# Optimization experiments

Measured on AMD Instinct MI355X. Metric: run time of the kernel, lower is better.

The kernel has to match this reference:

```python
import jax, jax.numpy as jnp
import numpy as np

N_EC, N_DG, N_CA3, N_CA1 = 100000, 400000, 120000, 100000
N_I_DG, N_I_CA3, N_I_CA1 = 10000, 3000, 2000
PP_NNZ, MF_NNZ, RC_NNZ, SC_NNZ = 10000000, 8000000, 6000000, 6000000
T, DT = 4, 0.5
A, B = 0.02, 0.2                      # Izhikevich a,b (same across subfields)
TAU_I, THR_I, INH_GAIN = 0.9, 1.0, 2.0  # inhibitory LIF params
IZH_CD = {'ec': (-65.0, 8.0), 'dg': (-65.0, 8.0), 'ca3': (-55.0, 4.0), 'ca1': (-65.0, 6.0)}


def _edges(key, n_src, n_tgt, nnz):
    # COO edge list matching init_sparse_projection: vals ~ N(0.5, 0.1), clamped >= 0
    k1, k2, k3 = jax.random.split(key, 3)
    src = jax.random.randint(k1, (nnz,), 0, n_src, dtype=jnp.int32)
    tgt = jax.random.randint(k2, (nnz,), 0, n_tgt, dtype=jnp.int32)
    val = jnp.clip(jax.random.normal(k3, (nnz,), jnp.float32) * 0.1 + 0.5, 0.0, None)
    return src, tgt, val


def _hetero(key, n, c, d):
    # per-neuron heterogeneity: c += 10 r^2, d -= 4 r^2, r ~ U(0,1)
    r = jax.random.uniform(key, (n,), jnp.float32)
    return jnp.float32(c) + 10.0 * r ** 2, jnp.float32(d) - 4.0 * r ** 2


def setup_inputs() -> dict:
    key = jax.random.key(0)
    ks = jax.random.split(key, 9)
    pp_src, pp_tgt, pp_val = _edges(ks[0], N_EC, N_DG, PP_NNZ)    # perforant path
    mf_src, mf_tgt, mf_val = _edges(ks[1], N_DG, N_CA3, MF_NNZ)   # mossy fibers
    rc_src, rc_tgt, rc_val = _edges(ks[2], N_CA3, N_CA3, RC_NNZ)  # CA3 recurrent
    sc_src, sc_tgt, sc_val = _edges(ks[3], N_CA3, N_CA1, SC_NNZ)  # Schaffer collaterals
    ec_c, ec_d = _hetero(ks[4], N_EC, *IZH_CD['ec'])
    dg_c, dg_d = _hetero(ks[5], N_DG, *IZH_CD['dg'])
    ca3_c, ca3_d = _hetero(ks[6], N_CA3, *IZH_CD['ca3'])
    ca1_c, ca1_d = _hetero(ks[7], N_CA1, *IZH_CD['ca1'])
    drive = jax.random.uniform(ks[8], (T, N_EC), jnp.float32) * 20.0  # input current, strong enough to spike
    return dict(drive=drive,
                pp_src=pp_src, pp_tgt=pp_tgt, pp_val=pp_val,
                mf_src=mf_src, mf_tgt=mf_tgt, mf_val=mf_val,
                rc_src=rc_src, rc_tgt=rc_tgt, rc_val=rc_val,
                sc_src=sc_src, sc_tgt=sc_tgt, sc_val=sc_val,
                ec_c=ec_c, ec_d=ec_d, dg_c=dg_c, dg_d=dg_d,
                ca3_c=ca3_c, ca3_d=ca3_d, ca1_c=ca1_c, ca1_d=ca1_d)


def reference(drive, pp_src, pp_tgt, pp_val, mf_src, mf_tgt, mf_val,
              rc_src, rc_tgt, rc_val, sc_src, sc_tgt, sc_val,
              ec_c, ec_d, dg_c, dg_d, ca3_c, ca3_d, ca1_c, ca1_d):

    def transmit(spk, src, tgt, val, n_tgt):
        # sparse_transmit: W^T @ spikes as gather + segment-scatter-add
        return jax.ops.segment_sum(val * spk[src], tgt, num_segments=n_tgt)

    def izh(v, u, c, d, I):
        v = jnp.clip(v + (0.04 * v * v + 5.0 * v + 140.0 - u + I) * DT, -90.0, 40.0)
        u = u + A * (B * v - u) * DT  # du uses post-update clamped v, as in torch
        s = (v >= 30.0).astype(jnp.float32)
        return jnp.where(s > 0, c, v), jnp.where(s > 0, u + d, u), s

    def lif(v, inp):
        v = TAU_I * v + (1.0 - TAU_I) * inp
        s = (v >= THR_I).astype(jnp.float32)
        return jnp.where(s > 0, 0.0, v), s

    def step(carry, I_ec):
        (ec_v, ec_u, dg_v, dg_u, c3_v, c3_u, c1_v, c1_u,
         c3_s, iv_dg, iv_c3, iv_c1) = carry
        # EC -> perforant path -> DG
        ec_v, ec_u, ec_s = izh(ec_v, ec_u, ec_c, ec_d, I_ec)
        dg_I = transmit(ec_s, pp_src, pp_tgt, pp_val, N_DG)
        iv_dg, is_dg = lif(iv_dg, jnp.full((N_I_DG,), dg_I.mean()))
        dg_v, dg_u, dg_s = izh(dg_v, dg_u, dg_c, dg_d, dg_I - INH_GAIN * is_dg.mean())
        # DG -> mossy fibers + CA3 recurrent -> CA3
        c3_I = (transmit(dg_s, mf_src, mf_tgt, mf_val, N_CA3)
                + transmit(c3_s, rc_src, rc_tgt, rc_val, N_CA3))
        iv_c3, is_c3 = lif(iv_c3, jnp.full((N_I_CA3,), c3_I.mean()))
        c3_v, c3_u, c3_s = izh(c3_v, c3_u, ca3_c, ca3_d, c3_I - INH_GAIN * is_c3.mean())
        # CA3 -> Schaffer collaterals -> CA1
        c1_I = transmit(c3_s, sc_src, sc_tgt, sc_val, N_CA1)
        iv_c1, is_c1 = lif(iv_c1, jnp.full((N_I_CA1,), c1_I.mean()))
        c1_v, c1_u, c1_s = izh(c1_v, c1_u, ca1_c, ca1_d, c1_I - INH_GAIN * is_c1.mean())
        carry = (ec_v, ec_u, dg_v, dg_u, c3_v, c3_u, c1_v, c1_u,
                 c3_s, iv_dg, iv_c3, iv_c1)
        return carry, c1_s

    f32 = jnp.float32
    init = (jnp.full((N_EC,), -65.0, f32), jnp.full((N_EC,), B * -65.0, f32),
            jnp.full((N_DG,), -65.0, f32), jnp.full((N_DG,), B * -65.0, f32),
            jnp.full((N_CA3,), -65.0, f32), jnp.full((N_CA3,), B * -65.0, f32),
            jnp.full((N_CA1,), -65.0, f32), jnp.full((N_CA1,), B * -65.0, f32),
            jnp.zeros((N_CA3,), f32),
            jnp.zeros((N_I_DG,), f32), jnp.zeros((N_I_CA3,), f32), jnp.zeros((N_I_CA1,), f32))
    carry, _ = jax.lax.scan(step, init, drive)
    return carry[6]  # final CA1 membrane potential, shape (N_CA1,)
```

## Files before the change

### kernel.cpp

```cpp
#include <hip/hip_runtime.h>


#define N_EC  100000
#define N_DG  400000
#define N_CA3 120000
#define N_CA1 100000

constexpr int PP_NNZ = 10000000, MF_NNZ = 8000000, RC_NNZ = 6000000, SC_NNZ = 6000000;
constexpr int T_STEPS = 4;

enum : size_t {
  OFF_EC_V = 0,
  OFF_EC_U = OFF_EC_V + N_EC,
  OFF_DG_V = OFF_EC_U + N_EC,
  OFF_DG_U = OFF_DG_V + N_DG,
  OFF_C3_V = OFF_DG_U + N_DG,
  OFF_C3_U = OFF_C3_V + N_CA3,
  OFF_C1_V = OFF_C3_U + N_CA3,
  OFF_C1_U = OFF_C1_V + N_CA1,
  OFF_DG_I = OFF_C1_U + N_CA1,
  OFF_C3_I = OFF_DG_I + N_DG,
  OFF_C1_I = OFF_C3_I + N_CA3,
  OFF_SCAL = OFF_C1_I + N_CA1,
  OFF_FLAG = OFF_SCAL + 64,
  OFF_MASK = OFF_FLAG + 64,
};
enum : size_t {
  MW_EC = 0,    MW_EC_N = 1600,
  MW_DG = 1600, MW_DG_N = 6272,
  MW_C3 = 7872, MW_C3_N = 1900,
  MW_TOT = 9772,
};

__global__ __launch_bounds__(256)
void init_kernel(float* __restrict__ ws) {
  int i0 = blockIdx.x * blockDim.x + threadIdx.x;
  int stride = gridDim.x * blockDim.x;
  int* flags = (int*)(ws + OFF_FLAG);
  unsigned long long* c3m = (unsigned long long*)(ws + OFF_MASK) + MW_C3;
  for (int j = i0; j < N_DG; j += stride) {
    ws[OFF_DG_V + j] = -65.0f; ws[OFF_DG_U + j] = -13.0f; ws[OFF_DG_I + j] = 0.0f;
    if (j < N_EC)  { ws[OFF_EC_V + j] = -65.0f; ws[OFF_EC_U + j] = -13.0f; }
    if (j < N_CA3) { ws[OFF_C3_V + j] = -65.0f; ws[OFF_C3_U + j] = -13.0f; ws[OFF_C3_I + j] = 0.0f; }
    if (j < N_CA1) { ws[OFF_C1_V + j] = -65.0f; ws[OFF_C1_U + j] = -13.0f; ws[OFF_C1_I + j] = 0.0f; }
    if (j < 64) ws[OFF_SCAL + j] = 0.0f;
    if (j < 16) flags[j] = 0;
    if (j < (int)MW_C3_N) c3m[j] = 0ull;
  }
}

__global__ __launch_bounds__(256)
void transmit_kernel(const int* __restrict__ src, const int* __restrict__ tgt,
                     const float* __restrict__ val,
                     const unsigned long long* __restrict__ mask,
                     float* __restrict__ I, float* __restrict__ sum_slot,
                     const int* __restrict__ flag, int nnz4)
{
  if (*flag == 0) return;
  float local = 0.0f;
  const int stride = gridDim.x * blockDim.x;
  for (int i = blockIdx.x * blockDim.x + threadIdx.x; i < nnz4; i += stride) {
    const int4   s4 = reinterpret_cast<const int4*>(src)[i];
    const int4   t4 = reinterpret_cast<const int4*>(tgt)[i];
    const float4 v4 = reinterpret_cast<const float4*>(val)[i];
    const int   ss[4] = {s4.x, s4.y, s4.z, s4.w};
    const int   tt[4] = {t4.x, t4.y, t4.z, t4.w};
    const float vv[4] = {v4.x, v4.y, v4.z, v4.w};
#pragma unroll
    for (int k = 0; k < 4; ++k) {
      if ((mask[ss[k] >> 6] >> (ss[k] & 63)) & 1ull) {
        atomicAdd(&I[tt[k]], vv[k]);
        local += vv[k];
      }
    }
  }
  for (int off = 32; off > 0; off >>= 1) local += __shfl_down(local, off);
  __shared__ float red[4];
  if ((threadIdx.x & 63) == 0) red[threadIdx.x >> 6] = local;
  __syncthreads();
  if (threadIdx.x == 0) {
    float bs = red[0] + red[1] + red[2] + red[3];
    if (bs != 0.0f) atomicAdd(sum_slot, bs);
  }
}

__device__ __forceinline__ void izh_step(float& vv, float& uu, float I,
                                         float c, float d, bool& s) {
  vv = vv + (0.04f * vv * vv + 5.0f * vv + 140.0f - uu + I) * 0.5f;
  vv = fminf(fmaxf(vv, -90.0f), 40.0f);
  uu = uu + 0.02f * (0.2f * vv - uu) * 0.5f;
  s = (vv >= 30.0f);
  if (s) { vv = c; uu = uu + d; }
}

__global__ __launch_bounds__(256)
void izh_ec_kernel(float* __restrict__ v, float* __restrict__ u,
                   const float* __restrict__ c, const float* __restrict__ d,
                   const float* __restrict__ drive,
                   unsigned long long* __restrict__ mask,
                   int* __restrict__ flag, int n)
{
  int i = blockIdx.x * blockDim.x + threadIdx.x;
  bool s = false;
  if (i < n) {
    float vv = v[i], uu = u[i];
    izh_step(vv, uu, drive[i], c[i], d[i], s);
    v[i] = vv; u[i] = uu;
  }
  unsigned long long m = __ballot(s);
  if ((threadIdx.x & 63) == 0) {
    mask[i >> 6] = m;
    if (m) atomicOr(flag, 1);
  }
}

__global__ __launch_bounds__(256)
void izh_lif_kernel(float* __restrict__ v, float* __restrict__ u,
                    const float* __restrict__ c, const float* __restrict__ d,
                    float* __restrict__ Ibuf,
                    const float* __restrict__ sum_slot,
                    const float* __restrict__ iv_prev, float* __restrict__ iv_next,
                    float inv_n,
                    unsigned long long* __restrict__ mask, int* __restrict__ flag,
                    float* __restrict__ out, int n)
{
  float mean = (*sum_slot) * inv_n;
  float ivn  = 0.9f * (*iv_prev) + 0.1f * mean;
  bool  lif_s = (ivn >= 1.0f);
  float inh   = lif_s ? 2.0f : 0.0f;
  if (blockIdx.x == 0 && threadIdx.x == 0) *iv_next = lif_s ? 0.0f : ivn;

  int i = blockIdx.x * blockDim.x + threadIdx.x;
  bool s = false;
  if (i < n) {
    float vv = v[i], uu = u[i];
    float I = Ibuf[i] - inh;
    Ibuf[i] = 0.0f;
    izh_step(vv, uu, I, c[i], d[i], s);
    v[i] = vv; u[i] = uu;
    if (out) out[i] = vv;
  }
  if (mask) {
    unsigned long long m = __ballot(s);
    if ((threadIdx.x & 63) == 0) {
      mask[i >> 6] = m;
      if (m) atomicOr(flag, 1);
    }
  }
}

extern "C" void kernel_launch(void* const* d_in, const int* in_sizes, int n_in,
                              void* d_out, int out_size, void* d_ws, size_t ws_size,
                              hipStream_t stream) {
  const float* drive  = (const float*)d_in[0];
  const int *pp_src = (const int*)d_in[1], *pp_tgt = (const int*)d_in[2];
  const float* pp_val = (const float*)d_in[3];
  const int *mf_src = (const int*)d_in[4], *mf_tgt = (const int*)d_in[5];
  const float* mf_val = (const float*)d_in[6];
  const int *rc_src = (const int*)d_in[7], *rc_tgt = (const int*)d_in[8];
  const float* rc_val = (const float*)d_in[9];
  const int *sc_src = (const int*)d_in[10], *sc_tgt = (const int*)d_in[11];
  const float* sc_val = (const float*)d_in[12];
  const float *ec_c = (const float*)d_in[13], *ec_d = (const float*)d_in[14];
  const float *dg_c = (const float*)d_in[15], *dg_d = (const float*)d_in[16];
  const float *c3_c = (const float*)d_in[17], *c3_d = (const float*)d_in[18];
  const float *c1_c = (const float*)d_in[19], *c1_d = (const float*)d_in[20];

  float* ws = (float*)d_ws;
  float* ec_v = ws + OFF_EC_V;  float* ec_u = ws + OFF_EC_U;
  float* dg_v = ws + OFF_DG_V;  float* dg_u = ws + OFF_DG_U;
  float* c3_v = ws + OFF_C3_V;  float* c3_u = ws + OFF_C3_U;
  float* c1_v = ws + OFF_C1_V;  float* c1_u = ws + OFF_C1_U;
  float* dg_I = ws + OFF_DG_I;  float* c3_I = ws + OFF_C3_I;  float* c1_I = ws + OFF_C1_I;
  float* scal = ws + OFF_SCAL;
  int*   flags = (int*)(ws + OFF_FLAG);
  unsigned long long* mbase = (unsigned long long*)(ws + OFF_MASK);
  unsigned long long* ec_m = mbase + MW_EC;
  unsigned long long* dg_m = mbase + MW_DG;
  unsigned long long* c3_m = mbase + MW_C3;

  float* out = (float*)d_out;
  auto grid = [](int n) { return (n + 255) / 256; };

  init_kernel<<<grid(N_DG), 256, 0, stream>>>(ws);

  for (int t = 0; t < T_STEPS; ++t) {
    float* sum_dg = &scal[t * 3 + 0];
    float* sum_c3 = &scal[t * 3 + 1];
    float* sum_c1 = &scal[t * 3 + 2];
    int* f_ec = &flags[t * 3 + 0];
    int* f_dg = &flags[t * 3 + 1];
    int* f_c3 = &flags[t * 3 + 2];
    int* f_c3_prev = (t == 0) ? &flags[15] : &flags[(t - 1) * 3 + 2];

    izh_ec_kernel<<<grid(N_EC), 256, 0, stream>>>(
        ec_v, ec_u, ec_c, ec_d, drive + (size_t)t * N_EC, ec_m, f_ec, N_EC);
    transmit_kernel<<<1024, 256, 0, stream>>>(
        pp_src, pp_tgt, pp_val, ec_m, dg_I, sum_dg, f_ec, PP_NNZ / 4);
    izh_lif_kernel<<<grid(N_DG), 256, 0, stream>>>(
        dg_v, dg_u, dg_c, dg_d, dg_I, sum_dg, &scal[16 + t], &scal[16 + t + 1],
        1.0f / (float)N_DG, dg_m, f_dg, nullptr, N_DG);
    transmit_kernel<<<1024, 256, 0, stream>>>(
        mf_src, mf_tgt, mf_val, dg_m, c3_I, sum_c3, f_dg, MF_NNZ / 4);
    transmit_kernel<<<1024, 256, 0, stream>>>(
        rc_src, rc_tgt, rc_val, c3_m, c3_I, sum_c3, f_c3_prev, RC_NNZ / 4);
    izh_lif_kernel<<<grid(N_CA3), 256, 0, stream>>>(
        c3_v, c3_u, c3_c, c3_d, c3_I, sum_c3, &scal[21 + t], &scal[21 + t + 1],
        1.0f / (float)N_CA3, c3_m, f_c3, nullptr, N_CA3);
    transmit_kernel<<<1024, 256, 0, stream>>>(
        sc_src, sc_tgt, sc_val, c3_m, c1_I, sum_c1, f_c3, SC_NNZ / 4);
    izh_lif_kernel<<<grid(N_CA1), 256, 0, stream>>>(
        c1_v, c1_u, c1_c, c1_d, c1_I, sum_c1, &scal[26 + t], &scal[26 + t + 1],
        1.0f / (float)N_CA1, nullptr, nullptr, out, N_CA1);
  }
}
```

Baseline: 326.0 us.

## Fuse whole simulation into one cooperative persistent kernel with grid syncs

Replaces the roughly 29 separate kernel launches per call with a single cooperative kernel of 512 blocks. Neuron state (v, u, c, d) lives in registers across time steps, and stages are separated by grid.sync instead of kernel boundaries. Grid syncs and zero-current reads are skipped when no spikes occurred. This is meant to remove launch overhead and repeated state loads and stores. In exchange it uses fewer threads for the atomic-heavy scatter loops, which can lower memory-level parallelism, and grid-wide barriers carry their own cost.

Measured after the change: 1.022 ms. +213.4%, slower.

```diff
diff --git a/kernel.cpp b/kernel.cpp
--- a/kernel.cpp
+++ b/kernel.cpp
@@ -1,4 +1,7 @@
 #include <hip/hip_runtime.h>
+#include <hip/hip_cooperative_groups.h>
+
+namespace cg = cooperative_groups;
 
 
 #define N_EC  100000
@@ -8,58 +11,51 @@
 
 constexpr int PP_NNZ = 10000000, MF_NNZ = 8000000, RC_NNZ = 6000000, SC_NNZ = 6000000;
 constexpr int T_STEPS = 4;
-
-enum : size_t {
-  OFF_EC_V = 0,
-  OFF_EC_U = OFF_EC_V + N_EC,
-  OFF_DG_V = OFF_EC_U + N_EC,
-  OFF_DG_U = OFF_DG_V + N_DG,
-  OFF_C3_V = OFF_DG_U + N_DG,
-  OFF_C3_U = OFF_C3_V + N_CA3,
-  OFF_C1_V = OFF_C3_U + N_CA3,
-  OFF_C1_U = OFF_C1_V + N_CA1,
-  OFF_DG_I = OFF_C1_U + N_CA1,
-  OFF_C3_I = OFF_DG_I + N_DG,
-  OFF_C1_I = OFF_C3_I + N_CA3,
-  OFF_SCAL = OFF_C1_I + N_CA1,
-  OFF_FLAG = OFF_SCAL + 64,
-  OFF_MASK = OFF_FLAG + 64,
+constexpr int NBLK = 512, TPB = 256;
+constexpr int NTH  = NBLK * TPB;
+constexpr int DGS  = (N_DG + NTH - 1) / NTH;
+
+constexpr size_t OFF_DG_I = 0;
+constexpr size_t OFF_C3_I = OFF_DG_I + N_DG;
+constexpr size_t OFF_C1_I = OFF_C3_I + N_CA3;
+constexpr size_t OFF_SUMS = OFF_C1_I + N_CA1;
+constexpr size_t OFF_FLAG = OFF_SUMS + 16;
+constexpr size_t OFF_MASK = OFF_FLAG + 16;
+constexpr size_t MW_EC = 0,    MW_EC_N = 1564;
+constexpr size_t MW_DG = 1564, MW_DG_N = 6250;
+constexpr size_t MW_C3 = 7814, MW_C3_N = 1876;
+
+struct SimParams {
+  const float* drive;
+  const int *pp_src, *pp_tgt; const float* pp_val;
+  const int *mf_src, *mf_tgt; const float* mf_val;
+  const int *rc_src, *rc_tgt; const float* rc_val;
+  const int *sc_src, *sc_tgt; const float* sc_val;
+  const float *ec_c, *ec_d, *dg_c, *dg_d, *c3_c, *c3_d, *c1_c, *c1_d;
+  float* out; float* ws;
 };
-enum : size_t {
-  MW_EC = 0,    MW_EC_N = 1600,
-  MW_DG = 1600, MW_DG_N = 6272,
-  MW_C3 = 7872, MW_C3_N = 1900,
-  MW_TOT = 9772,
-};
-
-__global__ __launch_bounds__(256)
-void init_kernel(float* __restrict__ ws) {
-  int i0 = blockIdx.x * blockDim.x + threadIdx.x;
-  int stride = gridDim.x * blockDim.x;
-  int* flags = (int*)(ws + OFF_FLAG);
-  unsigned long long* c3m = (unsigned long long*)(ws + OFF_MASK) + MW_C3;
-  for (int j = i0; j < N_DG; j += stride) {
-    ws[OFF_DG_V + j] = -65.0f; ws[OFF_DG_U + j] = -13.0f; ws[OFF_DG_I + j] = 0.0f;
-    if (j < N_EC)  { ws[OFF_EC_V + j] = -65.0f; ws[OFF_EC_U + j] = -13.0f; }
-    if (j < N_CA3) { ws[OFF_C3_V + j] = -65.0f; ws[OFF_C3_U + j] = -13.0f; ws[OFF_C3_I + j] = 0.0f; }
-    if (j < N_CA1) { ws[OFF_C1_V + j] = -65.0f; ws[OFF_C1_U + j] = -13.0f; ws[OFF_C1_I + j] = 0.0f; }
-    if (j < 64) ws[OFF_SCAL + j] = 0.0f;
-    if (j < 16) flags[j] = 0;
-    if (j < (int)MW_C3_N) c3m[j] = 0ull;
-  }
-}
-
-__global__ __launch_bounds__(256)
-void transmit_kernel(const int* __restrict__ src, const int* __restrict__ tgt,
-                     const float* __restrict__ val,
-                     const unsigned long long* __restrict__ mask,
-                     float* __restrict__ I, float* __restrict__ sum_slot,
-                     const int* __restrict__ flag, int nnz4)
-{
-  if (*flag == 0) return;
+
+__device__ __forceinline__ void izh_step(float& vv, float& uu, float I,
+                                         float c, float d, bool& s) {
+  vv = vv + (0.04f * vv * vv + 5.0f * vv + 140.0f - uu + I) * 0.5f;
+  vv = fminf(fmaxf(vv, -90.0f), 40.0f);
+  uu = uu + 0.02f * (0.2f * vv - uu) * 0.5f;
+  s = (vv >= 30.0f);
+  if (s) { vv = c; uu = uu + d; }
+}
+
+__device__ __forceinline__ float wave_sum(float x) {
+  for (int o = 32; o > 0; o >>= 1) x += __shfl_down(x, o);
+  return x;
+}
+
+__device__ void transmit(const int* __restrict__ src, const int* __restrict__ tgt,
+                         const float* __restrict__ val, int nnz4,
+                         const unsigned long long* __restrict__ mask,
+                         float* __restrict__ I, float* __restrict__ sum_slot,
+                         int tid) {
   float local = 0.0f;
-  const int stride = gridDim.x * blockDim.x;
-  for (int i = blockIdx.x * blockDim.x + threadIdx.x; i < nnz4; i += stride) {
+  for (int i = tid; i < nnz4; i += NTH) {
     const int4   s4 = reinterpret_cast<const int4*>(src)[i];
     const int4   t4 = reinterpret_cast<const int4*>(tgt)[i];
     const float4 v4 = reinterpret_cast<const float4*>(val)[i];
@@ -74,143 +70,155 @@
       }
     }
   }
-  for (int off = 32; off > 0; off >>= 1) local += __shfl_down(local, off);
-  __shared__ float red[4];
-  if ((threadIdx.x & 63) == 0) red[threadIdx.x >> 6] = local;
-  __syncthreads();
-  if (threadIdx.x == 0) {
-    float bs = red[0] + red[1] + red[2] + red[3];
-    if (bs != 0.0f) atomicAdd(sum_slot, bs);
-  }
-}
-
-__device__ __forceinline__ void izh_step(float& vv, float& uu, float I,
-                                         float c, float d, bool& s) {
-  vv = vv + (0.04f * vv * vv + 5.0f * vv + 140.0f - uu + I) * 0.5f;
-  vv = fminf(fmaxf(vv, -90.0f), 40.0f);
-  uu = uu + 0.02f * (0.2f * vv - uu) * 0.5f;
-  s = (vv >= 30.0f);
-  if (s) { vv = c; uu = uu + d; }
-}
-
-__global__ __launch_bounds__(256)
-void izh_ec_kernel(float* __restrict__ v, float* __restrict__ u,
-                   const float* __restrict__ c, const float* __restrict__ d,
-                   const float* __restrict__ drive,
-                   unsigned long long* __restrict__ mask,
-                   int* __restrict__ flag, int n)
-{
-  int i = blockIdx.x * blockDim.x + threadIdx.x;
-  bool s = false;
-  if (i < n) {
-    float vv = v[i], uu = u[i];
-    izh_step(vv, uu, drive[i], c[i], d[i], s);
-    v[i] = vv; u[i] = uu;
-  }
-  unsigned long long m = __ballot(s);
-  if ((threadIdx.x & 63) == 0) {
-    mask[i >> 6] = m;
-    if (m) atomicOr(flag, 1);
-  }
-}
-
-__global__ __launch_bounds__(256)
-void izh_lif_kernel(float* __restrict__ v, float* __restrict__ u,
-                    const float* __restrict__ c, const float* __restrict__ d,
-                    float* __restrict__ Ibuf,
-                    const float* __restrict__ sum_slot,
-                    const float* __restrict__ iv_prev, float* __restrict__ iv_next,
-                    float inv_n,
-                    unsigned long long* __restrict__ mask, int* __restrict__ flag,
-                    float* __restrict__ out, int n)
-{
-  float mean = (*sum_slot) * inv_n;
-  float ivn  = 0.9f * (*iv_prev) + 0.1f * mean;
-  bool  lif_s = (ivn >= 1.0f);
-  float inh   = lif_s ? 2.0f : 0.0f;
-  if (blockIdx.x == 0 && threadIdx.x == 0) *iv_next = lif_s ? 0.0f : ivn;
-
-  int i = blockIdx.x * blockDim.x + threadIdx.x;
-  bool s = false;
-  if (i < n) {
-    float vv = v[i], uu = u[i];
-    float I = Ibuf[i] - inh;
-    Ibuf[i] = 0.0f;
-    izh_step(vv, uu, I, c[i], d[i], s);
-    v[i] = vv; u[i] = uu;
-    if (out) out[i] = vv;
-  }
-  if (mask) {
-    unsigned long long m = __ballot(s);
-    if ((threadIdx.x & 63) == 0) {
-      mask[i >> 6] = m;
-      if (m) atomicOr(flag, 1);
-    }
-  }
-}
-
-extern "C" void kernel_launch(void* const* d_in, const int* in_sizes, int n_in,
-                              void* d_out, int out_size, void* d_ws, size_t ws_size,
-                              hipStream_t stream) {
-  const float* drive  = (const float*)d_in[0];
-  const int *pp_src = (const int*)d_in[1], *pp_tgt = (const int*)d_in[2];
-  const float* pp_val = (const float*)d_in[3];
-  const int *mf_src = (const int*)d_in[4], *mf_tgt = (const int*)d_in[5];
-  const float* mf_val = (const float*)d_in[6];
-  const int *rc_src = (const int*)d_in[7], *rc_tgt = (const int*)d_in[8];
-  const float* rc_val = (const float*)d_in[9];
-  const int *sc_src = (const int*)d_in[10], *sc_tgt = (const int*)d_in[11];
-  const float* sc_val = (const float*)d_in[12];
-  const float *ec_c = (const float*)d_in[13], *ec_d = (const float*)d_in[14];
-  const float *dg_c = (const float*)d_in[15], *dg_d = (const float*)d_in[16];
-  const float *c3_c = (const float*)d_in[17], *c3_d = (const float*)d_in[18];
-  const float *c1_c = (const float*)d_in[19], *c1_d = (const float*)d_in[20];
-
-  float* ws = (float*)d_ws;
-  float* ec_v = ws + OFF_EC_V;  float* ec_u = ws + OFF_EC_U;
-  float* dg_v = ws + OFF_DG_V;  float* dg_u = ws + OFF_DG_U;
-  float* c3_v = ws + OFF_C3_V;  float* c3_u = ws + OFF_C3_U;
-  float* c1_v = ws + OFF_C1_V;  float* c1_u = ws + OFF_C1_U;
-  float* dg_I = ws + OFF_DG_I;  float* c3_I = ws + OFF_C3_I;  float* c1_I = ws + OFF_C1_I;
-  float* scal = ws + OFF_SCAL;
+  local = wave_sum(local);
+  if ((threadIdx.x & 63) == 0 && local != 0.0f) atomicAdd(sum_slot, local);
+}
+
+__global__ __launch_bounds__(TPB, 2)
+void sim_kernel(SimParams p) {
+  cg::grid_group grid = cg::this_grid();
+  const int tid  = blockIdx.x * blockDim.x + threadIdx.x;
+  const int lane = threadIdx.x & 63;
+
+  float* ws   = p.ws;
+  float* dg_I = ws + OFF_DG_I;
+  float* c3_I = ws + OFF_C3_I;
+  float* c1_I = ws + OFF_C1_I;
+  float* sums = ws + OFF_SUMS;
   int*   flags = (int*)(ws + OFF_FLAG);
   unsigned long long* mbase = (unsigned long long*)(ws + OFF_MASK);
   unsigned long long* ec_m = mbase + MW_EC;
   unsigned long long* dg_m = mbase + MW_DG;
   unsigned long long* c3_m = mbase + MW_C3;
 
-  float* out = (float*)d_out;
-  auto grid = [](int n) { return (n + 255) / 256; };
-
-  init_kernel<<<grid(N_DG), 256, 0, stream>>>(ws);
+  for (int i = tid; i < N_DG;  i += NTH) dg_I[i] = 0.0f;
+  for (int i = tid; i < N_CA3; i += NTH) c3_I[i] = 0.0f;
+  for (int i = tid; i < N_CA1; i += NTH) c1_I[i] = 0.0f;
+  if (tid < 16) { sums[tid] = 0.0f; flags[tid] = 0; }
+
+  const bool ec_ok = tid < N_EC;
+  float ecv = -65.0f, ecu = -13.0f, ecc = 0.0f, ecd = 0.0f;
+  if (ec_ok) { ecc = p.ec_c[tid]; ecd = p.ec_d[tid]; }
+
+  float dgv[DGS], dgu[DGS], dgc[DGS], dgd[DGS];
+#pragma unroll
+  for (int k = 0; k < DGS; ++k) {
+    int idx = tid + k * NTH;
+    dgv[k] = -65.0f; dgu[k] = -13.0f; dgc[k] = 0.0f; dgd[k] = 0.0f;
+    if (idx < N_DG) { dgc[k] = p.dg_c[idx]; dgd[k] = p.dg_d[idx]; }
+  }
+  const bool c3_ok = tid < N_CA3;
+  float c3v = -65.0f, c3u = -13.0f, c3c = 0.0f, c3dd = 0.0f;
+  if (c3_ok) { c3c = p.c3_c[tid]; c3dd = p.c3_d[tid]; }
+  const bool c1_ok = tid < N_CA1;
+  float c1v = -65.0f, c1u = -13.0f, c1c = 0.0f, c1dd = 0.0f;
+  if (c1_ok) { c1c = p.c1_c[tid]; c1dd = p.c1_d[tid]; }
+
+  float iv_dg = 0.0f, iv_c3 = 0.0f, iv_c1 = 0.0f;
+
+  grid.sync();
 
   for (int t = 0; t < T_STEPS; ++t) {
-    float* sum_dg = &scal[t * 3 + 0];
-    float* sum_c3 = &scal[t * 3 + 1];
-    float* sum_c1 = &scal[t * 3 + 2];
-    int* f_ec = &flags[t * 3 + 0];
-    int* f_dg = &flags[t * 3 + 1];
-    int* f_c3 = &flags[t * 3 + 2];
-    int* f_c3_prev = (t == 0) ? &flags[15] : &flags[(t - 1) * 3 + 2];
-
-    izh_ec_kernel<<<grid(N_EC), 256, 0, stream>>>(
-        ec_v, ec_u, ec_c, ec_d, drive + (size_t)t * N_EC, ec_m, f_ec, N_EC);
-    transmit_kernel<<<1024, 256, 0, stream>>>(
-        pp_src, pp_tgt, pp_val, ec_m, dg_I, sum_dg, f_ec, PP_NNZ / 4);
-    izh_lif_kernel<<<grid(N_DG), 256, 0, stream>>>(
-        dg_v, dg_u, dg_c, dg_d, dg_I, sum_dg, &scal[16 + t], &scal[16 + t + 1],
-        1.0f / (float)N_DG, dg_m, f_dg, nullptr, N_DG);
-    transmit_kernel<<<1024, 256, 0, stream>>>(
-        mf_src, mf_tgt, mf_val, dg_m, c3_I, sum_c3, f_dg, MF_NNZ / 4);
-    transmit_kernel<<<1024, 256, 0, stream>>>(
-        rc_src, rc_tgt, rc_val, c3_m, c3_I, sum_c3, f_c3_prev, RC_NNZ / 4);
-    izh_lif_kernel<<<grid(N_CA3), 256, 0, stream>>>(
-        c3_v, c3_u, c3_c, c3_d, c3_I, sum_c3, &scal[21 + t], &scal[21 + t + 1],
-        1.0f / (float)N_CA3, c3_m, f_c3, nullptr, N_CA3);
-    transmit_kernel<<<1024, 256, 0, stream>>>(
-        sc_src, sc_tgt, sc_val, c3_m, c1_I, sum_c1, f_c3, SC_NNZ / 4);
-    izh_lif_kernel<<<grid(N_CA1), 256, 0, stream>>>(
-        c1_v, c1_u, c1_c, c1_d, c1_I, sum_c1, &scal[26 + t], &scal[26 + t + 1],
-        1.0f / (float)N_CA1, nullptr, nullptr, out, N_CA1);
+    {
+      bool s = false;
+      if (ec_ok) izh_step(ecv, ecu, p.drive[(size_t)t * N_EC + tid], ecc, ecd, s);
+      unsigned long long m = __ballot(s);
+      if (lane == 0 && ec_ok) {
+        ec_m[tid >> 6] = m;
+        if (m) atomicOr(&flags[t * 3 + 0], 1);
+      }
+    }
+    grid.sync();
+    const int fe = flags[t * 3 + 0];
+    if (fe) {
+      transmit(p.pp_src, p.pp_tgt, p.pp_val, PP_NNZ / 4, ec_m, dg_I, &sums[t * 3 + 0], tid);
+      grid.sync();
+    }
+    {
+      float mean = sums[t * 3 + 0] * (1.0f / (float)N_DG);
+      iv_dg = 0.9f * iv_dg + 0.1f * mean;
+      bool ls = (iv_dg >= 1.0f);
+      float inh = ls ? 2.0f : 0.0f;
+      if (ls) iv_dg = 0.0f;
+#pragma unroll
+      for (int k = 0; k < DGS; ++k) {
+        int idx = tid + k * NTH;
+        bool s = false;
+        if (idx < N_DG) {
+          float I = (fe ? dg_I[idx] : 0.0f) - inh;
+          if (fe) dg_I[idx] = 0.0f;
+          izh_step(dgv[k], dgu[k], I, dgc[k], dgd[k], s);
+        }
+        unsigned long long m = __ballot(s);
+        if (lane == 0 && idx < N_DG) {
+          dg_m[idx >> 6] = m;
+          if (m) atomicOr(&flags[t * 3 + 1], 1);
+        }
+      }
+    }
+    grid.sync();
+    const int fd  = flags[t * 3 + 1];
+    const int fcp = (t > 0) ? flags[(t - 1) * 3 + 2] : 0;
+    if (fd)  transmit(p.mf_src, p.mf_tgt, p.mf_val, MF_NNZ / 4, dg_m, c3_I, &sums[t * 3 + 1], tid);
+    if (fcp) transmit(p.rc_src, p.rc_tgt, p.rc_val, RC_NNZ / 4, c3_m, c3_I, &sums[t * 3 + 1], tid);
+    if (fd | fcp) grid.sync();
+    {
+      float mean = sums[t * 3 + 1] * (1.0f / (float)N_CA3);
+      iv_c3 = 0.9f * iv_c3 + 0.1f * mean;
+      bool ls = (iv_c3 >= 1.0f);
+      float inh = ls ? 2.0f : 0.0f;
+      if (ls) iv_c3 = 0.0f;
+      bool s = false;
+      if (c3_ok) {
+        float I = ((fd | fcp) ? c3_I[tid] : 0.0f) - inh;
+        if (fd | fcp) c3_I[tid] = 0.0f;
+        izh_step(c3v, c3u, I, c3c, c3dd, s);
+      }
+      unsigned long long m = __ballot(s);
+      if (lane == 0 && c3_ok) {
+        c3_m[tid >> 6] = m;
+        if (m) atomicOr(&flags[t * 3 + 2], 1);
+      }
+    }
+    grid.sync();
+    const int fc = flags[t * 3 + 2];
+    if (fc) {
+      transmit(p.sc_src, p.sc_tgt, p.sc_val, SC_NNZ / 4, c3_m, c1_I, &sums[t * 3 + 2], tid);
+      grid.sync();
+    }
+    {
+      float mean = sums[t * 3 + 2] * (1.0f / (float)N_CA1);
+      iv_c1 = 0.9f * iv_c1 + 0.1f * mean;
+      bool ls = (iv_c1 >= 1.0f);
+      float inh = ls ? 2.0f : 0.0f;
+      if (ls) iv_c1 = 0.0f;
+      if (c1_ok) {
+        float I = (fc ? c1_I[tid] : 0.0f) - inh;
+        if (fc) c1_I[tid] = 0.0f;
+        bool s = false;
+        izh_step(c1v, c1u, I, c1c, c1dd, s);
+        if (t == T_STEPS - 1) p.out[tid] = c1v;
+      }
+    }
   }
 }
+
+extern "C" void kernel_launch(void* const* d_in, const int* in_sizes, int n_in,
+                              void* d_out, int out_size, void* d_ws, size_t ws_size,
+                              hipStream_t stream) {
+  SimParams prm;
+  prm.drive  = (const float*)d_in[0];
+  prm.pp_src = (const int*)d_in[1];  prm.pp_tgt = (const int*)d_in[2];  prm.pp_val = (const float*)d_in[3];
+  prm.mf_src = (const int*)d_in[4];  prm.mf_tgt = (const int*)d_in[5];  prm.mf_val = (const float*)d_in[6];
+  prm.rc_src = (const int*)d_in[7];  prm.rc_tgt = (const int*)d_in[8];  prm.rc_val = (const float*)d_in[9];
+  prm.sc_src = (const int*)d_in[10]; prm.sc_tgt = (const int*)d_in[11]; prm.sc_val = (const float*)d_in[12];
+  prm.ec_c = (const float*)d_in[13]; prm.ec_d = (const float*)d_in[14];
+  prm.dg_c = (const float*)d_in[15]; prm.dg_d = (const float*)d_in[16];
+  prm.c3_c = (const float*)d_in[17]; prm.c3_d = (const float*)d_in[18];
+  prm.c1_c = (const float*)d_in[19]; prm.c1_d = (const float*)d_in[20];
+  prm.out = (float*)d_out;
+  prm.ws  = (float*)d_ws;
+
+  void* args[] = { &prm };
+  hipLaunchCooperativeKernel((void*)sim_kernel, dim3(NBLK), dim3(TPB), args, 0, stream);
+}
```
